# Optimization experiments

Measured on AMD Instinct MI355X. Metric: run time of the kernel, lower is better.

## Reference

```python
import jax, jax.numpy as jnp
import numpy as np

LN_EPS = 1e-5


def setup_inputs() -> dict:
    key = jax.random.key(0)
    ks = jax.random.split(key, 12)
    B, T, U, H, V = 4, 512, 128, 512, 41
    src = jax.random.normal(ks[0], (B, T, H), dtype=jnp.float32)
    tgt = jax.random.normal(ks[1], (B, U, H), dtype=jnp.float32)
    src_len = jax.random.randint(ks[2], (B,), 1, T + 1, dtype=jnp.int32)
    tgt_len = jax.random.randint(ks[3], (B,), 1, U + 1, dtype=jnp.int32)
    s = 1.0 / np.sqrt(H)
    W1 = jax.random.uniform(ks[4], (H, H), jnp.float32, -s, s)
    b1 = jax.random.uniform(ks[5], (H,), jnp.float32, -s, s)
    W2 = jax.random.uniform(ks[6], (H, H), jnp.float32, -s, s)
    b2 = jax.random.uniform(ks[7], (H,), jnp.float32, -s, s)
    ln_g = jnp.ones((H,), jnp.float32)
    ln_b = jnp.zeros((H,), jnp.float32)
    Wl = jax.random.uniform(ks[8], (H, V), jnp.float32, -s, s)
    bl = jax.random.uniform(ks[9], (V,), jnp.float32, -s, s)
    return dict(source_encodings=src, source_lengths=src_len,
                target_encodings=tgt, target_lengths=tgt_len,
                W1=W1, b1=b1, W2=W2, b2=b2, ln_g=ln_g, ln_b=ln_b,
                Wl=Wl, bl=bl)


def _f_target(tgt, W1, b1, W2, b2, ln_g, ln_b):
    h = jax.nn.gelu(tgt @ W1 + b1, approximate=False)  # exact GELU (torch default)
    h = h @ W2 + b2
    mu = jnp.mean(h, axis=-1, keepdims=True)
    var = jnp.var(h, axis=-1, keepdims=True)
    return (h - mu) * jax.lax.rsqrt(var + LN_EPS) * ln_g + ln_b


def reference(source_encodings, source_lengths, target_encodings, target_lengths,
              W1, b1, W2, b2, ln_g, ln_b, Wl, bl):
    tgt = _f_target(target_encodings, W1, b1, W2, b2, ln_g, ln_b)  # [B,U,H]
    # joint broadcast add: [B,T,1,H] + [B,1,U,H] -> [B,T,U,H]
    joint = source_encodings[:, :, None, :] + tgt[:, None, :, :]
    act = jnp.tanh(joint)
    out = act @ Wl + bl  # [B,T,U,V]
    return out, source_lengths, target_lengths
```

## Files before the change

kernel.cpp:

```cpp
#include <hip/hip_runtime.h>
#include <math.h>

#define Bb 4
#define Tt 512
#define Uu 128
#define Hh 512
#define Vv 41

typedef __attribute__((ext_vector_type(8))) short short8;
typedef __attribute__((ext_vector_type(4))) float f32x4;
typedef __attribute__((ext_vector_type(2))) float v2f;

__device__ __forceinline__ unsigned pack_bf16_rne(float hi, float lo) {
    unsigned xh = __float_as_uint(hi); xh += 0x7fffu + ((xh >> 16) & 1u);
    unsigned xl = __float_as_uint(lo); xl += 0x7fffu + ((xl >> 16) & 1u);
    return __builtin_amdgcn_perm(xh, xl, 0x07060302);
}

__device__ __forceinline__ unsigned short bf16_rne(float v) {
    unsigned x = __float_as_uint(v);
    x += 0x7fffu + ((x >> 16) & 1u);
    return (unsigned short)(x >> 16);
}

__device__ __forceinline__ float bf16lo(unsigned u) { return __uint_as_float(u << 16); }
__device__ __forceinline__ float bf16hi(unsigned u) { return __uint_as_float(u & 0xffff0000u); }

__device__ __forceinline__ unsigned tanh2_pack(float x0, float x1) {
    v2f xc;
    xc.x = __builtin_amdgcn_fmed3f(x0, -3.0f, 3.0f);
    xc.y = __builtin_amdgcn_fmed3f(x1, -3.0f, 3.0f);
    v2f t = xc * xc;
    v2f p = t * (v2f){-0.00140725f, -0.00140725f} + (v2f){0.0288922f, 0.0288922f};
    p = p * t + (v2f){-0.2177528f, -0.2177528f};
    p = p * t + (v2f){0.9707868f, 0.9707868f};
    v2f g = xc * p;
    return __builtin_amdgcn_perm(__float_as_uint(g.y), __float_as_uint(g.x), 0x07060302);
}

__global__ __launch_bounds__(256) void prep_pack(
    const float* __restrict__ W1, const float* __restrict__ W2,
    const float* __restrict__ Wl, const float* __restrict__ tgt,
    unsigned short* __restrict__ Wp1, unsigned short* __restrict__ Wp2,
    unsigned short* __restrict__ Wpl, unsigned short* __restrict__ tgtA,
    const int* __restrict__ sl, const int* __restrict__ tl,
    float* __restrict__ lenDst)
{
    __shared__ __align__(16) char smem[16640];
    const int bid = blockIdx.x, tid = threadIdx.x;

    if (bid >= 136) {
        unsigned short (*At)[520] = (unsigned short (*)[520])smem;
        const int rt = bid - 136;
        const float4* t4 = (const float4*)(tgt + (size_t)rt * 16 * Hh);
        #pragma unroll
        for (int j = 0; j < 8; ++j) {
            int fi = j * 256 + tid;
            int row = fi >> 7, c4 = fi & 127;
            float4 v = t4[fi];
            uint2 pk;
            pk.x = pack_bf16_rne(v.y, v.x);
            pk.y = pack_bf16_rne(v.w, v.z);
            *(uint2*)&At[row][c4 * 4] = pk;
        }
        __syncthreads();
        #pragma unroll
        for (int i = 0; i < 4; ++i) {
            int chunk = i * 256 + tid;
            int ks = chunk >> 6, l = chunk & 63;
            int q = l >> 4, nc = l & 15;
            short8 v = *(const short8*)&At[nc][ks * 32 + q * 8];
            *(short8*)(tgtA + ((size_t)(rt * 16 + ks) * 64 + l) * 8) = v;
        }
        return;
    }

    if (bid == 135 && tid < 2 * Bb)
        lenDst[tid] = (tid < Bb) ? (float)sl[tid] : (float)tl[tid - Bb];

    float (*T)[65] = (float (*)[65])smem;
    const float* Wsrc; unsigned short* Wdst; int k0, n0, isWl;
    if (bid < 64)       { Wsrc = W1; Wdst = Wp1; k0 = (bid >> 3) * 64; n0 = (bid & 7) * 64; isWl = 0; }
    else if (bid < 128) { Wsrc = W2; Wdst = Wp2; k0 = ((bid - 64) >> 3) * 64; n0 = ((bid - 64) & 7) * 64; isWl = 0; }
    else                { Wsrc = Wl; Wdst = Wpl; k0 = (bid - 128) * 64; n0 = 0; isWl = 1; }

    #pragma unroll
    for (int i = 0; i < 16; ++i) {
        int idx = i * 256 + tid;
        int kk = idx >> 6, nn = idx & 63;
        float v;
        if (isWl) v = (nn < Vv) ? Wl[(k0 + kk) * Vv + nn] : 0.0f;
        else      v = Wsrc[(size_t)(k0 + kk) * 512 + n0 + nn];
        T[kk][nn] = v;
    }
    __syncthreads();

    #pragma unroll
    for (int i = 0; i < 2; ++i) {
        int task = i * 256 + tid;
        int nn = task & 63, kg = task >> 6;
        if (isWl && nn >= 48) continue;
        int n = n0 + nn, k = k0 + kg * 8;
        float e[8];
        #pragma unroll
        for (int j = 0; j < 8; ++j) e[j] = T[kg * 8 + j][nn];
        uint4 pk;
        pk.x = pack_bf16_rne(e[1], e[0]);
        pk.y = pack_bf16_rne(e[3], e[2]);
        pk.z = pack_bf16_rne(e[5], e[4]);
        pk.w = pack_bf16_rne(e[7], e[6]);
        int ntg = n >> 4, ncol = n & 15;
        int ks = (k >> 5) & 15, quad = (k >> 3) & 3;
        int lane = quad * 16 + ncol;
        *(uint4*)(Wdst + (size_t)((ntg * 16 + ks) * 64 + lane) * 8) = pk;
    }
}

__global__ __launch_bounds__(128) void gemm_t1(
    const unsigned short* __restrict__ tgtA,
    const unsigned short* __restrict__ Wp1, const float* __restrict__ b1,
    unsigned short* __restrict__ h1A)
{
    __shared__ unsigned short At[16][72];
    const int nb = blockIdx.x, rt = blockIdx.y;
    const int tid = threadIdx.x, lane = tid & 63, w = tid >> 6;
    const int ncol = lane & 15, quad = lane >> 4;
    const int nt0 = nb * 4 + w * 2;

    const unsigned short* ap = tgtA + ((size_t)rt * 1024 + lane) * 8;
    const unsigned short* bp = Wp1 + (size_t)lane * 8;

    f32x4 acc0 = (f32x4){0.f,0.f,0.f,0.f}, acc1 = (f32x4){0.f,0.f,0.f,0.f};
    short8 ac  = *(const short8*)(ap);
    short8 b0c = *(const short8*)(bp + (size_t)nt0 * 8192);
    short8 b1c = *(const short8*)(bp + (size_t)(nt0 + 1) * 8192);

    #pragma unroll
    for (int ks = 0; ks < 16; ++ks) {
        short8 an, b0n, b1n;
        if (ks < 15) {
            an  = *(const short8*)(ap + (ks + 1) * 512);
            b0n = *(const short8*)(bp + (size_t)nt0 * 8192 + (ks + 1) * 512);
            b1n = *(const short8*)(bp + (size_t)(nt0 + 1) * 8192 + (ks + 1) * 512);
        }
        acc0 = __builtin_amdgcn_mfma_f32_16x16x32_bf16(ac, b0c, acc0, 0, 0, 0);
        acc1 = __builtin_amdgcn_mfma_f32_16x16x32_bf16(ac, b1c, acc1, 0, 0, 0);
        ac = an; b0c = b0n; b1c = b1n;
    }

    #pragma unroll
    for (int nt = 0; nt < 2; ++nt) {
        int n = nb * 64 + w * 32 + nt * 16 + ncol;
        float bias = b1[n];
        f32x4 A = nt ? acc1 : acc0;
        #pragma unroll
        for (int r = 0; r < 4; ++r) {
            float v = A[r] + bias;
            float g = 0.5f * v * (1.0f + erff(v * 0.70710678118654752f));
            At[quad * 4 + r][w * 32 + nt * 16 + ncol] = bf16_rne(g);
        }
    }
    __syncthreads();

    {
        int l = lane;
        short8 v = *(const short8*)&At[l & 15][w * 32 + (l >> 4) * 8];
        int ksg = nb * 2 + w;
        *(short8*)(h1A + ((size_t)(rt * 16 + ksg) * 64 + l) * 8) = v;
    }
}

__global__ __launch_bounds__(512) void gemm_t2ln(
    const unsigned short* __restrict__ h1A,
    const unsigned short* __restrict__ Wp2, const float* __restrict__ b2,
    const float* __restrict__ ln_g, const float* __restrict__ ln_b,
    unsigned short* __restrict__ tgtPb)
{
    __shared__ float Ct[16][520];
    const int rt = blockIdx.x;
    const int tid = threadIdx.x, lane = tid & 63, w = tid >> 6;
    const int ncol = lane & 15, quad = lane >> 4;
    const int nt0 = w * 4;

    const unsigned short* ap = h1A + ((size_t)rt * 1024 + lane) * 8;
    const unsigned short* bp = Wp2 + (size_t)lane * 8 + (size_t)nt0 * 8192;

    f32x4 acc[4];
    #pragma unroll
    for (int i = 0; i < 4; ++i) acc[i] = (f32x4){0.f, 0.f, 0.f, 0.f};

    short8 ac = *(const short8*)(ap);
    short8 bc[4];
    #pragma unroll
    for (int i = 0; i < 4; ++i) bc[i] = *(const short8*)(bp + (size_t)i * 8192);

    #pragma unroll
    for (int ks = 0; ks < 16; ++ks) {
        short8 an, bn[4];
        if (ks < 15) {
            an = *(const short8*)(ap + (ks + 1) * 512);
            #pragma unroll
            for (int i = 0; i < 4; ++i)
                bn[i] = *(const short8*)(bp + (size_t)i * 8192 + (ks + 1) * 512);
        }
        #pragma unroll
        for (int i = 0; i < 4; ++i)
            acc[i] = __builtin_amdgcn_mfma_f32_16x16x32_bf16(ac, bc[i], acc[i], 0, 0, 0);
        ac = an;
        #pragma unroll
        for (int i = 0; i < 4; ++i) bc[i] = bn[i];
    }

    #pragma unroll
    for (int nt = 0; nt < 4; ++nt) {
        int n = w * 64 + nt * 16 + ncol;
        float bias = b2[n];
        #pragma unroll
        for (int r = 0; r < 4; ++r)
            Ct[quad * 4 + r][n] = acc[nt][r] + bias;
    }
    __syncthreads();

    #pragma unroll
    for (int rr = 0; rr < 2; ++rr) {
        const int row = w * 2 + rr;
        const float4* cr = (const float4*)&Ct[row][0];
        float4 v0 = cr[lane], v1 = cr[lane + 64];
        float s = v0.x + v0.y + v0.z + v0.w + v1.x + v1.y + v1.z + v1.w;
        float q = v0.x*v0.x + v0.y*v0.y + v0.z*v0.z + v0.w*v0.w
                + v1.x*v1.x + v1.y*v1.y + v1.z*v1.z + v1.w*v1.w;
        #pragma unroll
        for (int off = 32; off > 0; off >>= 1) {
            s += __shfl_xor(s, off, 64);
            q += __shfl_xor(q, off, 64);
        }
        float mu = s * (1.0f / Hh);
        float rs = rsqrtf(q * (1.0f / Hh) - mu * mu + 1e-5f);

        const int r = rt * 16 + row;
        const int bb = r >> 7, u = r & 127;
        #pragma unroll
        for (int j = 0; j < 2; ++j) {
            int k0 = j * 256 + lane * 4;
            float4 v = j ? v1 : v0;
            float4 g4 = ((const float4*)ln_g)[j * 64 + lane];
            float4 b4 = ((const float4*)ln_b)[j * 64 + lane];
            float4 o;
            o.x = (v.x - mu) * rs * g4.x + b4.x;
            o.y = (v.y - mu) * rs * g4.y + b4.y;
            o.z = (v.z - mu) * rs * g4.z + b4.z;
            o.w = (v.w - mu) * rs * g4.w + b4.w;
            uint2 pk;
            pk.x = pack_bf16_rne(o.y, o.x);
            pk.y = pack_bf16_rne(o.w, o.z);
            int chunk = k0 >> 3, half = (k0 >> 2) & 1;
            *(uint2*)(tgtPb + ((size_t)(bb * 64 + chunk) * 128 + u) * 8 + half * 4) = pk;
        }
    }
}

__global__ __launch_bounds__(256) void joint_mfma(
    const float* __restrict__ src, const unsigned short* __restrict__ tgtPb,
    const unsigned short* __restrict__ Wpl, const float* __restrict__ bl,
    float* __restrict__ out)
{
    __shared__ float srcl[2 * Hh];

    const int t0 = blockIdx.x * 2, b = blockIdx.y, uh = blockIdx.z;
    const int tid = threadIdx.x;
    const int lane = tid & 63, wave = tid >> 6;
    const int ncol = lane & 15, quad = lane >> 4;

    const float4* s4 = (const float4*)(src + ((size_t)(b * Tt + t0)) * Hh);
    ((float4*)srcl)[tid] = s4[tid];

    const int u0 = uh * 64 + (wave & 1) * 32 + ncol;
    const unsigned short* pA = tgtPb + (size_t)b * 65536;
    const unsigned short* bp = Wpl + (size_t)lane * 8;

    uint4 Aa[2], Ac[2];
    short8 Bq[2][3];
    {
        const unsigned short* p0 = pA + ((size_t)(0 * 4 + quad) * 128) * 8;
        Aa[0] = *(const uint4*)(p0 + u0 * 8);
        Ac[0] = *(const uint4*)(p0 + (u0 + 16) * 8);
        Bq[0][0] = *(const short8*)(bp);
        Bq[0][1] = *(const short8*)(bp + 8192);
        Bq[0][2] = *(const short8*)(bp + 16384);
        const unsigned short* p1 = pA + ((size_t)(1 * 4 + quad) * 128) * 8;
        Aa[1] = *(const uint4*)(p1 + u0 * 8);
        Ac[1] = *(const uint4*)(p1 + (u0 + 16) * 8);
        Bq[1][0] = *(const short8*)(bp + 512);
        Bq[1][1] = *(const short8*)(bp + 8192 + 512);
        Bq[1][2] = *(const short8*)(bp + 16384 + 512);
    }

    f32x4 acc[2][3];
    #pragma unroll
    for (int nt = 0; nt < 3; ++nt) {
        int n = nt * 16 + ncol;
        float bv = (n < Vv) ? bl[n] : 0.0f;
        acc[0][nt] = (f32x4){bv, bv, bv, bv};
        acc[1][nt] = (f32x4){bv, bv, bv, bv};
    }

    __syncthreads();
    const float* srow = srcl + (wave >> 1) * Hh;
    float4 sA = *(const float4*)(srow + quad * 8);
    float4 sB = *(const float4*)(srow + quad * 8 + 4);

    #pragma unroll
    for (int ks = 0; ks < 16; ++ks) {
        const int st = ks & 1;
        uint4 a = Aa[st], c = Ac[st];
        short8 B0 = Bq[st][0], B1 = Bq[st][1], B2 = Bq[st][2];

        if (ks + 2 < 16) {
            const unsigned short* pn = pA + ((size_t)((ks + 2) * 4 + quad) * 128) * 8;
            Aa[st] = *(const uint4*)(pn + u0 * 8);
            Ac[st] = *(const uint4*)(pn + (u0 + 16) * 8);
            Bq[st][0] = *(const short8*)(bp + (ks + 2) * 512);
            Bq[st][1] = *(const short8*)(bp + 8192 + (ks + 2) * 512);
            Bq[st][2] = *(const short8*)(bp + 16384 + (ks + 2) * 512);
        }
        float4 nsA, nsB;
        if (ks < 15) {
            nsA = *(const float4*)(srow + (ks + 1) * 32 + quad * 8);
            nsB = *(const float4*)(srow + (ks + 1) * 32 + quad * 8 + 4);
        }

        union { uint4 u; short8 s; } f0, f1;
        f0.u.x = tanh2_pack(sA.x + bf16lo(a.x), sA.y + bf16hi(a.x));
        f0.u.y = tanh2_pack(sA.z + bf16lo(a.y), sA.w + bf16hi(a.y));
        f0.u.z = tanh2_pack(sB.x + bf16lo(a.z), sB.y + bf16hi(a.z));
        f0.u.w = tanh2_pack(sB.z + bf16lo(a.w), sB.w + bf16hi(a.w));
        f1.u.x = tanh2_pack(sA.x + bf16lo(c.x), sA.y + bf16hi(c.x));
        f1.u.y = tanh2_pack(sA.z + bf16lo(c.y), sA.w + bf16hi(c.y));
        f1.u.z = tanh2_pack(sB.x + bf16lo(c.z), sB.y + bf16hi(c.z));
        f1.u.w = tanh2_pack(sB.z + bf16lo(c.w), sB.w + bf16hi(c.w));

        acc[0][0] = __builtin_amdgcn_mfma_f32_16x16x32_bf16(f0.s, B0, acc[0][0], 0, 0, 0);
        acc[1][0] = __builtin_amdgcn_mfma_f32_16x16x32_bf16(f1.s, B0, acc[1][0], 0, 0, 0);
        acc[0][1] = __builtin_amdgcn_mfma_f32_16x16x32_bf16(f0.s, B1, acc[0][1], 0, 0, 0);
        acc[1][1] = __builtin_amdgcn_mfma_f32_16x16x32_bf16(f1.s, B1, acc[1][1], 0, 0, 0);
        acc[0][2] = __builtin_amdgcn_mfma_f32_16x16x32_bf16(f0.s, B2, acc[0][2], 0, 0, 0);
        acc[1][2] = __builtin_amdgcn_mfma_f32_16x16x32_bf16(f1.s, B2, acc[1][2], 0, 0, 0);

        sA = nsA; sB = nsB;
    }

    const int t = t0 + (wave >> 1);
    const int ub = uh * 64 + (wave & 1) * 32;
    float* ob = out + ((size_t)(b * Tt + t)) * Uu * Vv;
    #pragma unroll
    for (int mi = 0; mi < 2; ++mi) {
        #pragma unroll
        for (int nt = 0; nt < 3; ++nt) {
            int n = nt * 16 + ncol;
            if (n < Vv) {
                #pragma unroll
                for (int r = 0; r < 4; ++r) {
                    int m = ub + mi * 16 + quad * 4 + r;
                    ob[m * Vv + n] = acc[mi][nt][r];
                }
            }
        }
    }
}

extern "C" void kernel_launch(void* const* d_in, const int* in_sizes, int n_in,
                              void* d_out, int out_size, void* d_ws, size_t ws_size,
                              hipStream_t stream)
{
    const float* src  = (const float*)d_in[0];
    const int*   slen = (const int*)  d_in[1];
    const float* tgt  = (const float*)d_in[2];
    const int*   tlen = (const int*)  d_in[3];
    const float* W1   = (const float*)d_in[4];
    const float* b1   = (const float*)d_in[5];
    const float* W2   = (const float*)d_in[6];
    const float* b2   = (const float*)d_in[7];
    const float* ln_g = (const float*)d_in[8];
    const float* ln_b = (const float*)d_in[9];
    const float* Wl   = (const float*)d_in[10];
    const float* bl   = (const float*)d_in[11];

    float* out = (float*)d_out;
    char* ws = (char*)d_ws;
    unsigned short* tgtPb = (unsigned short*)(ws);
    unsigned short* Wp1   = (unsigned short*)(ws + 524288);
    unsigned short* Wp2   = (unsigned short*)(ws + 1048576);
    unsigned short* Wpl   = (unsigned short*)(ws + 1572864);
    unsigned short* tgtA  = (unsigned short*)(ws + 1638400);
    unsigned short* h1A   = (unsigned short*)(ws + 2162688);

    hipLaunchKernelGGL(prep_pack, dim3(168), dim3(256), 0, stream,
                       W1, W2, Wl, tgt, Wp1, Wp2, Wpl, tgtA,
                       slen, tlen, out + (size_t)Bb * Tt * Uu * Vv);
    hipLaunchKernelGGL(gemm_t1, dim3(8, 32), dim3(128), 0, stream,
                       tgtA, Wp1, b1, h1A);
    hipLaunchKernelGGL(gemm_t2ln, dim3(32), dim3(512), 0, stream,
                       h1A, Wp2, b2, ln_g, ln_b, tgtPb);
    hipLaunchKernelGGL(joint_mfma, dim3(Tt / 2, Bb, 2), dim3(256), 0, stream,
                       src, tgtPb, Wpl, bl, out);
}
```

Baseline: 142.9 us.

## Use tanh addition identity to replace per-element polynomial tanh in joint

After: 142.4 us. Within noise of the previous version (-0.3%).

```diff
diff --git a/kernel.cpp b/kernel.cpp
--- a/kernel.cpp
+++ b/kernel.cpp
@@ -26,15 +26,19 @@
 __device__ __forceinline__ float bf16lo(unsigned u) { return __uint_as_float(u << 16); }
 __device__ __forceinline__ float bf16hi(unsigned u) { return __uint_as_float(u & 0xffff0000u); }
 
-__device__ __forceinline__ unsigned tanh2_pack(float x0, float x1) {
-    v2f xc;
-    xc.x = __builtin_amdgcn_fmed3f(x0, -3.0f, 3.0f);
-    xc.y = __builtin_amdgcn_fmed3f(x1, -3.0f, 3.0f);
-    v2f t = xc * xc;
-    v2f p = t * (v2f){-0.00140725f, -0.00140725f} + (v2f){0.0288922f, 0.0288922f};
-    p = p * t + (v2f){-0.2177528f, -0.2177528f};
-    p = p * t + (v2f){0.9707868f, 0.9707868f};
-    v2f g = xc * p;
+__device__ __forceinline__ float tanh_acc(float x) {
+    float e = __expf(2.0f * x);
+    return 1.0f - 2.0f * __builtin_amdgcn_rcpf(e + 1.0f);
+}
+
+__device__ __forceinline__ unsigned mob2(unsigned aw, float ts0, float ts1) {
+    v2f tt = {bf16lo(aw), bf16hi(aw)};
+    v2f ts = {ts0, ts1};
+    v2f nm = ts + tt;
+    v2f dn = ts * tt + (v2f){1.f, 1.f};
+    v2f g;
+    g.x = nm.x * __builtin_amdgcn_rcpf(dn.x);
+    g.y = nm.y * __builtin_amdgcn_rcpf(dn.y);
     return __builtin_amdgcn_perm(__float_as_uint(g.y), __float_as_uint(g.x), 0x07060302);
 }
 
@@ -246,10 +250,10 @@
             float4 g4 = ((const float4*)ln_g)[j * 64 + lane];
             float4 b4 = ((const float4*)ln_b)[j * 64 + lane];
             float4 o;
-            o.x = (v.x - mu) * rs * g4.x + b4.x;
-            o.y = (v.y - mu) * rs * g4.y + b4.y;
-            o.z = (v.z - mu) * rs * g4.z + b4.z;
-            o.w = (v.w - mu) * rs * g4.w + b4.w;
+            o.x = tanh_acc((v.x - mu) * rs * g4.x + b4.x);
+            o.y = tanh_acc((v.y - mu) * rs * g4.y + b4.y);
+            o.z = tanh_acc((v.z - mu) * rs * g4.z + b4.z);
+            o.w = tanh_acc((v.w - mu) * rs * g4.w + b4.w);
             uint2 pk;
             pk.x = pack_bf16_rne(o.y, o.x);
             pk.y = pack_bf16_rne(o.w, o.z);
@@ -271,8 +275,13 @@
     const int lane = tid & 63, wave = tid >> 6;
     const int ncol = lane & 15, quad = lane >> 4;
 
-    const float4* s4 = (const float4*)(src + ((size_t)(b * Tt + t0)) * Hh);
-    ((float4*)srcl)[tid] = s4[tid];
+    {
+        const float4* s4 = (const float4*)(src + ((size_t)(b * Tt + t0)) * Hh);
+        float4 v = s4[tid];
+        v.x = tanh_acc(v.x); v.y = tanh_acc(v.y);
+        v.z = tanh_acc(v.z); v.w = tanh_acc(v.w);
+        ((float4*)srcl)[tid] = v;
+    }
 
     const int u0 = uh * 64 + (wave & 1) * 32 + ncol;
     const unsigned short* pA = tgtPb + (size_t)b * 65536;
@@ -330,14 +339,14 @@
         }
 
         union { uint4 u; short8 s; } f0, f1;
-        f0.u.x = tanh2_pack(sA.x + bf16lo(a.x), sA.y + bf16hi(a.x));
-        f0.u.y = tanh2_pack(sA.z + bf16lo(a.y), sA.w + bf16hi(a.y));
-        f0.u.z = tanh2_pack(sB.x + bf16lo(a.z), sB.y + bf16hi(a.z));
-        f0.u.w = tanh2_pack(sB.z + bf16lo(a.w), sB.w + bf16hi(a.w));
-        f1.u.x = tanh2_pack(sA.x + bf16lo(c.x), sA.y + bf16hi(c.x));
-        f1.u.y = tanh2_pack(sA.z + bf16lo(c.y), sA.w + bf16hi(c.y));
-        f1.u.z = tanh2_pack(sB.x + bf16lo(c.z), sB.y + bf16hi(c.z));
-        f1.u.w = tanh2_pack(sB.z + bf16lo(c.w), sB.w + bf16hi(c.w));
+        f0.u.x = mob2(a.x, sA.x, sA.y);
+        f0.u.y = mob2(a.y, sA.z, sA.w);
+        f0.u.z = mob2(a.z, sB.x, sB.y);
+        f0.u.w = mob2(a.w, sB.z, sB.w);
+        f1.u.x = mob2(c.x, sA.x, sA.y);
+        f1.u.y = mob2(c.y, sA.z, sA.w);
+        f1.u.z = mob2(c.z, sB.x, sB.y);
+        f1.u.w = mob2(c.w, sB.z, sB.w);
 
         acc[0][0] = __builtin_amdgcn_mfma_f32_16x16x32_bf16(f0.s, B0, acc[0][0], 0, 0, 0);
         acc[1][0] = __builtin_amdgcn_mfma_f32_16x16x32_bf16(f1.s, B0, acc[1][0], 0, 0, 0);
```
